# Kernel tuning notes

Measured on AMD Instinct MI355X. Metric: run time of the kernel, lower is better.

## Reference

```python
import jax, jax.numpy as jnp
import numpy as np

EPS = 1e-5
NO_ACT = 3

def _causal_conv(x, w, b, dil):
    # x: [B, Cin, T], w: [Cout, Cin, K]; left-pad by (K-1)*dil == Conv1d(pad)+Chomp1d
    pad = (w.shape[2] - 1) * dil
    y = jax.lax.conv_general_dilated(x, w, window_strides=(1,), padding=[(pad, 0)],
                                     rhs_dilation=(dil,), dimension_numbers=("NCH", "OIH", "NCH"))
    return y + b[None, :, None]

def _bn(x, g, bt, m, v):
    # eval-mode BatchNorm1d over channel dim
    return (x - m[None, :, None]) * (g / jnp.sqrt(v + EPS))[None, :, None] + bt[None, :, None]

def _block(x, w1, b1, w2, b2, g1, bt1, m1, v1, g2, bt2, m2, v2, dil, dw=None, db=None):
    out = jax.nn.relu(_bn(_causal_conv(x, w1, b1, dil), g1, bt1, m1, v1))
    out = jax.nn.relu(_bn(_causal_conv(out, w2, b2, dil), g2, bt2, m2, v2))
    res = x if dw is None else _causal_conv(x, dw, db, 1)
    return jax.nn.relu(out + res)

def _logits(x, c0w1, c0b1, c0w2, c0b2, c0g1, c0bt1, c0m1, c0v1, c0g2, c0bt2, c0m2, c0v2, c0dw, c0db,
            c1w1, c1b1, c1w2, c1b2, c1g1, c1bt1, c1m1, c1v1, c1g2, c1bt2, c1m2, c1v2, aw, ab, lw, lb):
    h = jnp.swapaxes(x, 1, 2)  # [B, Cin, T]
    h = _block(h, c0w1, c0b1, c0w2, c0b2, c0g1, c0bt1, c0m1, c0v1, c0g2, c0bt2, c0m2, c0v2, 1, c0dw, c0db)
    h = _block(h, c1w1, c1b1, c1w2, c1b2, c1g1, c1bt1, c1m1, c1v1, c1g2, c1bt2, c1m2, c1v2, 2)
    z = jnp.swapaxes(h, 1, 2)  # [B, T, C]
    attn = jax.nn.sigmoid(z @ aw + ab)  # [B, T, 1]
    return (z * attn) @ lw + lb  # [B, T, 5]

def setup_inputs():
    key = jax.random.key(0)
    ks = iter(jax.random.split(key, 64))
    B, T, CIN, C, K, NC = 32, 4096, 34, 256, 3, 5
    def conv_w(co, ci, k):
        return jax.random.normal(next(ks), (co, ci, k), jnp.float32) * np.float32(np.sqrt(2.0 / (ci * k)))
    def vec(n, kind="randn"):
        if kind == "randn":
            return jax.random.normal(next(ks), (n,), jnp.float32) * 0.1
        return jax.random.uniform(next(ks), (n,), jnp.float32, 0.5, 1.5)
    inp = {"x": jax.random.normal(next(ks), (B, T, CIN), jnp.float32)}
    for i, ci in [(0, CIN), (1, C)]:
        inp[f"c{i}w1"] = conv_w(C, ci, K); inp[f"c{i}b1"] = vec(C)
        inp[f"c{i}w2"] = conv_w(C, C, K); inp[f"c{i}b2"] = vec(C)
        for j in (1, 2):
            inp[f"c{i}g{j}"] = 1.0 + vec(C)
            inp[f"c{i}bt{j}"] = vec(C)
            inp[f"c{i}m{j}"] = vec(C)
            inp[f"c{i}v{j}"] = vec(C, "rand")
    inp["c0dw"] = conv_w(C, CIN, 1); inp["c0db"] = vec(C)
    inp["aw"] = jax.random.normal(next(ks), (C, 1), jnp.float32) * np.float32(np.sqrt(1.0 / C))
    inp["ab"] = vec(1)
    inp["lw"] = jax.random.normal(next(ks), (C, NC), jnp.float32) * np.float32(np.sqrt(1.0 / C))
    inp["lb"] = vec(NC)
    return inp

def reference(x, c0w1, c0b1, c0w2, c0b2, c0g1, c0bt1, c0m1, c0v1, c0g2, c0bt2, c0m2, c0v2, c0dw, c0db,
              c1w1, c1b1, c1w2, c1b2, c1g1, c1bt1, c1m1, c1v1, c1g2, c1bt2, c1m2, c1v2, aw, ab, lw, lb):
    logits = _logits(x, c0w1, c0b1, c0w2, c0b2, c0g1, c0bt1, c0m1, c0v1, c0g2, c0bt2, c0m2, c0v2, c0dw, c0db,
                     c1w1, c1b1, c1w2, c1b2, c1g1, c1bt1, c1m1, c1v1, c1g2, c1bt2, c1m2, c1v2, aw, ab, lw, lb)
    probs = jax.nn.softmax(logits, axis=-1)
    B, T, NC = probs.shape
    preds = jnp.argmax(probs, axis=-1).astype(jnp.int32)
    # --- conservative no-activity: clipped window (size 5) majority check ---
    non3 = (preds != NO_ACT).astype(jnp.int32)
    cs = jnp.concatenate([jnp.zeros((B, 1), jnp.int32), jnp.cumsum(non3, axis=1)], axis=1)  # [B, T+1]
    t = jnp.arange(T)
    start = jnp.maximum(0, t - 2)
    end = jnp.minimum(T, t + 3)
    wsum = cs[:, end] - cs[:, start]          # non-no-activity count in window, [B, T]
    wlen = (end - start)[None, :]
    alt = jnp.argmax(probs.at[:, :, NO_ACT].set(0.0), axis=-1).astype(jnp.int32)
    proc = jnp.where((preds == NO_ACT) & (2 * wsum > wlen), alt, preds)
    # --- transition rules: sequential state smoothing scan over time ---
    TM = jnp.ones((5, 5), jnp.float32).at[1, 2].set(0.0).at[2, 0].set(0.0)
    def step(prev, inp):
        curr, p = inp                          # curr: [B] int32, p: [B, 5]
        mask = TM[prev]                        # allowed next-states, [B, 5]
        invalid = jnp.take_along_axis(mask, curr[:, None], axis=1)[:, 0] == 0
        vp = p * mask
        cand = jnp.where(vp.sum(-1) == 0, prev, jnp.argmax(vp, axis=-1).astype(jnp.int32))
        new = jnp.where(invalid, cand, curr)
        return new, new
    init = proc[:, 0]
    _, rest = jax.lax.scan(step, init, (proc[:, 1:].T, jnp.swapaxes(probs[:, 1:], 0, 1)))
    processed = jnp.concatenate([init[:, None], rest.T], axis=1)  # [B, T]
    return logits, processed
```

## Files before the change

kernel.cpp:

```cpp
#include <hip/hip_runtime.h>
#include <hip/hip_bf16.h>


#define T_LEN 4096
#define CIN   34
#define EPSV  1e-5f
#define HALO  16
#define TT    48
#define TW    64
#define NTILE 86

__device__ __forceinline__ int hswz(int row, int col) {
    return row * TW + ((((col >> 2) ^ ((row >> 3) & 15)) << 2) | (col & 3));
}
__device__ __forceinline__ float4* lds_ptr4(float* buf, int row, int col) {
    return (float4*)&buf[row * TW + (((col >> 2) ^ ((row >> 3) & 15)) << 2)];
}
__device__ __forceinline__ float4 lds_read4(const float* buf, int row, int col) {
    return *(const float4*)&buf[row * TW + (((col >> 2) ^ ((row >> 3) & 15)) << 2)];
}

__device__ __forceinline__ void bs_load(const float* __restrict__ wraw, int ch,
                                        float4 r[3], int tid) {
    #pragma unroll
    for (int k = 0; k < 3; ++k) {
        int s = tid + k * 512;
        int co = s / 6, q = s - co * 6;
        r[k] = *(const float4*)&wraw[co * 768 + ch * 24 + q * 4];
    }
}
__device__ __forceinline__ void bs_write(float* wch, const float4 r[3], int tid) {
    #pragma unroll
    for (int k = 0; k < 3; ++k) {
        int s = tid + k * 512;
        int co = s / 6, q = s - co * 6;
        wch[(q * 4 + 0) * 256 + co] = r[k].x;
        wch[(q * 4 + 1) * 256 + co] = r[k].y;
        wch[(q * 4 + 2) * 256 + co] = r[k].z;
        wch[(q * 4 + 3) * 256 + co] = r[k].w;
    }
}

__device__ __forceinline__ void s1_load(const float* __restrict__ w1, int ch,
                                        float r[12], int tid) {
    int nrows = (ch < 4) ? 24 : 6;
    int slots = nrows * 256;
    #pragma unroll
    for (int k = 0; k < 12; ++k) {
        int s = tid + k * 512;
        if (s < slots) {
            int co = s / nrows, kr = s - co * nrows;
            r[k] = w1[co * 102 + ch * 24 + kr];
        }
    }
}
__device__ __forceinline__ void s1_write(float* wch, int ch, const float r[12], int tid) {
    int nrows = (ch < 4) ? 24 : 6;
    int slots = nrows * 256;
    #pragma unroll
    for (int k = 0; k < 12; ++k) {
        int s = tid + k * 512;
        if (s < slots) {
            int co = s / nrows, kr = s - co * nrows;
            wch[kr * 256 + co] = r[k];
        }
    }
}

__device__ __forceinline__ void ds_stage(float* wch, const float* __restrict__ dw,
                                         int ch, int tid) {
    int nci = (ch < 4) ? 8 : 2;
    int slots = nci * 256;
    #pragma unroll
    for (int k = 0; k < 4; ++k) {
        int s = tid + k * 512;
        if (s < slots) {
            int ci_l = s % nci, co = s / nci;
            wch[ci_l * 256 + co] = dw[co * CIN + ch * 8 + ci_l];
        }
    }
}

template <int DIL>
__device__ __forceinline__ void chunk_compute(const float* src, const float* wch,
                                              int rowBase, int KH, int co0, int c0,
                                              float (&acc)[8][16]) {
    const int cL = (c0 >= 4) ? c0 - 4 : 0;
    #pragma unroll
    for (int rep = 0; rep < 2; ++rep) {
        int ci_l = KH + rep * 4;
        int row = rowBase + ci_l;
        float rw[20];
        *(float4*)&rw[0]  = lds_read4(src, row, cL);
        *(float4*)&rw[4]  = lds_read4(src, row, c0);
        *(float4*)&rw[8]  = lds_read4(src, row, c0 + 4);
        *(float4*)&rw[12] = lds_read4(src, row, c0 + 8);
        *(float4*)&rw[16] = lds_read4(src, row, c0 + 12);
        #pragma unroll
        for (int kk = 0; kk < 3; ++kk) {
            float wv[8];
            *(float4*)&wv[0] = *(const float4*)&wch[(ci_l * 3 + kk) * 256 + co0];
            *(float4*)&wv[4] = *(const float4*)&wch[(ci_l * 3 + kk) * 256 + co0 + 4];
            const int off = (DIL == 2) ? 2 * kk : kk + 2;
            #pragma unroll
            for (int i = 0; i < 8; ++i)
                #pragma unroll
                for (int j = 0; j < 16; ++j)
                    acc[i][j] += wv[i] * rw[j + off];
        }
    }
}

__device__ __forceinline__ void chunk_compute_x(const float* __restrict__ x,
                                                const float* wch, int b, int t0,
                                                int ciBase, int nci, int KH,
                                                int co0, int c0, float (&acc)[8][16]) {
    #pragma unroll
    for (int rep = 0; rep < 2; ++rep) {
        int ci_l = KH + rep * 4;
        if (ci_l < nci) {
            int ci = ciBase + ci_l;
            float rw[20];
            rw[0] = 0.f; rw[1] = 0.f;
            #pragma unroll
            for (int idx = 2; idx < 20; ++idx) {
                int t = t0 - HALO + c0 + idx - 4;
                rw[idx] = (t >= 0 && t < T_LEN) ? x[(b * T_LEN + t) * CIN + ci] : 0.f;
            }
            #pragma unroll
            for (int kk = 0; kk < 3; ++kk) {
                float wv[8];
                *(float4*)&wv[0] = *(const float4*)&wch[(ci_l * 3 + kk) * 256 + co0];
                *(float4*)&wv[4] = *(const float4*)&wch[(ci_l * 3 + kk) * 256 + co0 + 4];
                #pragma unroll
                for (int i = 0; i < 8; ++i)
                    #pragma unroll
                    for (int j = 0; j < 16; ++j)
                        acc[i][j] += wv[i] * rw[j + kk + 2];
            }
        }
    }
}

__device__ __forceinline__ void chunk_compute_ds(const float* __restrict__ x,
                                                 const float* wch, int b, int t0,
                                                 int ciBase, int nci, int KH,
                                                 int co0, int c0, float (&acc)[8][16]) {
    #pragma unroll
    for (int rep = 0; rep < 2; ++rep) {
        int ci_l = KH + rep * 4;
        if (ci_l < nci) {
            int ci = ciBase + ci_l;
            float xv[16];
            #pragma unroll
            for (int j = 0; j < 16; ++j) {
                int t = t0 - HALO + c0 + j;
                xv[j] = (t >= 0 && t < T_LEN) ? x[(b * T_LEN + t) * CIN + ci] : 0.f;
            }
            float wv[8];
            *(float4*)&wv[0] = *(const float4*)&wch[ci_l * 256 + co0];
            *(float4*)&wv[4] = *(const float4*)&wch[ci_l * 256 + co0 + 4];
            #pragma unroll
            for (int i = 0; i < 8; ++i)
                #pragma unroll
                for (int j = 0; j < 16; ++j)
                    acc[i][j] += wv[i] * xv[j];
        }
    }
}

__device__ __forceinline__ void kh_store(float* tgt, float (&acc)[8][16], int co0, int c0) {
    #pragma unroll
    for (int i = 0; i < 8; ++i)
        #pragma unroll
        for (int j4 = 0; j4 < 4; ++j4)
            *lds_ptr4(tgt, co0 + i, c0 + j4 * 4) =
                make_float4(acc[i][j4*4+0], acc[i][j4*4+1], acc[i][j4*4+2], acc[i][j4*4+3]);
}
__device__ __forceinline__ void kh_add(float* tgt, float (&acc)[8][16], int co0, int c0) {
    #pragma unroll
    for (int i = 0; i < 8; ++i)
        #pragma unroll
        for (int j4 = 0; j4 < 4; ++j4) {
            float4* p = lds_ptr4(tgt, co0 + i, c0 + j4 * 4);
            float4 pv = *p;
            pv.x += acc[i][j4*4+0]; pv.y += acc[i][j4*4+1];
            pv.z += acc[i][j4*4+2]; pv.w += acc[i][j4*4+3];
            *p = pv;
        }
}
__device__ __forceinline__ void kh_final0(float* tgt, float (&acc)[8][16],
                                          const float* __restrict__ g,  const float* __restrict__ bt,
                                          const float* __restrict__ m,  const float* __restrict__ v,
                                          const float* __restrict__ bb,
                                          int co0, int c0, int t0) {
    #pragma unroll
    for (int i = 0; i < 8; ++i) {
        int co = co0 + i;
        float sc = g[co] / sqrtf(v[co] + EPSV);
        float bi = (bb[co] - m[co]) * sc + bt[co];
        #pragma unroll
        for (int j4 = 0; j4 < 4; ++j4) {
            float4* p = lds_ptr4(tgt, co, c0 + j4 * 4);
            float4 pv = *p;
            float pr[4] = {pv.x, pv.y, pv.z, pv.w};
            float o[4];
            #pragma unroll
            for (int r = 0; r < 4; ++r) {
                float s = (pr[r] + acc[i][j4*4+r]) * sc + bi;
                o[r] = fmaxf(s, 0.f);
                int t = t0 - HALO + c0 + j4 * 4 + r;
                if (t < 0) o[r] = 0.f;
            }
            *p = make_float4(o[0], o[1], o[2], o[3]);
        }
    }
}
__device__ __forceinline__ void kh_res2(float* tgt, float (&acc)[8][16],
                                        const float* __restrict__ db,
                                        int co0, int c0, int t0) {
    #pragma unroll
    for (int i = 0; i < 8; ++i) {
        float d = db[co0 + i];
        #pragma unroll
        for (int j4 = 0; j4 < 4; ++j4) {
            float4* p = lds_ptr4(tgt, co0 + i, c0 + j4 * 4);
            float4 pv = *p;
            float pr[4] = {pv.x, pv.y, pv.z, pv.w};
            float o[4];
            #pragma unroll
            for (int r = 0; r < 4; ++r) {
                float s = pr[r] + acc[i][j4*4+r] + d;
                o[r] = fmaxf(s, 0.f);
                int t = t0 - HALO + c0 + j4 * 4 + r;
                if (t < 0) o[r] = 0.f;
            }
            *p = make_float4(o[0], o[1], o[2], o[3]);
        }
    }
}

#define ZERO_ACC() { _Pragma("unroll") for (int i = 0; i < 8; ++i) \
                     _Pragma("unroll") for (int j = 0; j < 16; ++j) acc[i][j] = 0.f; }

#define REDUCE0(TGT, G, BT, M, V, BB) {                         \
    __syncthreads();                                            \
    if (KH == 3) kh_store(TGT, acc, co0, c0);                   \
    __syncthreads();                                            \
    if (KH == 2) kh_add(TGT, acc, co0, c0);                     \
    __syncthreads();                                            \
    if (KH == 1) kh_add(TGT, acc, co0, c0);                     \
    __syncthreads();                                            \
    if (KH == 0) kh_final0(TGT, acc, G, BT, M, V, BB, co0, c0, t0); \
    __syncthreads(); }

#define REDUCE_RES(TGT, DB) {                                   \
    __syncthreads();                                            \
    if (KH == 3) kh_add(TGT, acc, co0, c0);                     \
    __syncthreads();                                            \
    if (KH == 2) kh_add(TGT, acc, co0, c0);                     \
    __syncthreads();                                            \
    if (KH == 1) kh_add(TGT, acc, co0, c0);                     \
    __syncthreads();                                            \
    if (KH == 0) kh_res2(TGT, acc, DB, co0, c0, t0);            \
    __syncthreads(); }

__global__ __launch_bounds__(512, 2) void tcn_fused(
    const float* __restrict__ x,
    const float* __restrict__ c0w1, const float* __restrict__ c0b1,
    const float* __restrict__ c0w2, const float* __restrict__ c0b2,
    const float* __restrict__ c0g1, const float* __restrict__ c0bt1,
    const float* __restrict__ c0m1, const float* __restrict__ c0v1,
    const float* __restrict__ c0g2, const float* __restrict__ c0bt2,
    const float* __restrict__ c0m2, const float* __restrict__ c0v2,
    const float* __restrict__ c1w1, const float* __restrict__ c1b1,
    const float* __restrict__ c1w2, const float* __restrict__ c1b2,
    const float* __restrict__ c1g1, const float* __restrict__ c1bt1,
    const float* __restrict__ c1m1, const float* __restrict__ c1v1,
    const float* __restrict__ c1g2, const float* __restrict__ c1bt2,
    const float* __restrict__ c1m2, const float* __restrict__ c1v2,
    const float* __restrict__ c0dw, const float* __restrict__ c0db,
    const float* __restrict__ aw,   const float* __restrict__ ab,
    const float* __restrict__ lw,   const float* __restrict__ lb,
    float* __restrict__ out)
{
    __shared__ float bufA[256 * TW];
    __shared__ float bufB[256 * TW];
    __shared__ float wch[24 * 256];

    const int b   = blockIdx.y;
    const int t0  = blockIdx.x * TT;
    const int tid = threadIdx.x;
    const int CG  = tid & 31, sg = tid >> 5;
    const int TG  = sg & 3,  KH = sg >> 2;
    const int co0 = CG * 8,  c0 = TG * 16;

    float acc[8][16];

    ZERO_ACC();
    {
        float r[12];
        s1_load(c0w1, 0, r, tid);
        for (int ch = 0; ch < 5; ++ch) {
            __syncthreads();
            s1_write(wch, ch, r, tid);
            __syncthreads();
            if (ch + 1 < 5) s1_load(c0w1, ch + 1, r, tid);
            chunk_compute_x(x, wch, b, t0, ch * 8, (ch < 4) ? 8 : 2, KH, co0, c0, acc);
        }
    }
    REDUCE0(bufA, c0g1, c0bt1, c0m1, c0v1, c0b1);

    ZERO_ACC();
    {
        float4 r4[3];
        bs_load(c0w2, 0, r4, tid);
        for (int ch = 0; ch < 32; ++ch) {
            __syncthreads();
            bs_write(wch, r4, tid);
            __syncthreads();
            if (ch + 1 < 32) bs_load(c0w2, ch + 1, r4, tid);
            chunk_compute<1>(bufA, wch, ch * 8, KH, co0, c0, acc);
        }
    }
    REDUCE0(bufB, c0g2, c0bt2, c0m2, c0v2, c0b2);

    ZERO_ACC();
    for (int ch = 0; ch < 5; ++ch) {
        __syncthreads();
        ds_stage(wch, c0dw, ch, tid);
        __syncthreads();
        chunk_compute_ds(x, wch, b, t0, ch * 8, (ch < 4) ? 8 : 2, KH, co0, c0, acc);
    }
    REDUCE_RES(bufB, c0db);

    ZERO_ACC();
    {
        float4 r4[3];
        bs_load(c1w1, 0, r4, tid);
        for (int ch = 0; ch < 32; ++ch) {
            __syncthreads();
            bs_write(wch, r4, tid);
            __syncthreads();
            if (ch + 1 < 32) bs_load(c1w1, ch + 1, r4, tid);
            chunk_compute<2>(bufB, wch, ch * 8, KH, co0, c0, acc);
        }
    }
    REDUCE0(bufA, c1g1, c1bt1, c1m1, c1v1, c1b1);

    ZERO_ACC();
    {
        float4 r4[3];
        bs_load(c1w2, 0, r4, tid);
        for (int ch = 0; ch < 32; ++ch) {
            __syncthreads();
            bs_write(wch, r4, tid);
            __syncthreads();
            if (ch + 1 < 32) bs_load(c1w2, ch + 1, r4, tid);
            chunk_compute<2>(bufA, wch, ch * 8, KH, co0, c0, acc);
        }
    }
    REDUCE0(bufA, c1g2, c1bt2, c1m2, c1v2, c1b2);

    {
        #pragma unroll
        for (int ii = 0; ii < 2; ++ii) {
            int co = co0 + KH * 2 + ii;
            #pragma unroll
            for (int j4 = 0; j4 < 4; ++j4) {
                float4* p = lds_ptr4(bufA, co, c0 + j4 * 4);
                float4 a = *p;
                float4 rr = lds_read4(bufB, co, c0 + j4 * 4);
                a.x = fmaxf(a.x + rr.x, 0.f);
                a.y = fmaxf(a.y + rr.y, 0.f);
                a.z = fmaxf(a.z + rr.z, 0.f);
                a.w = fmaxf(a.w + rr.w, 0.f);
                *p = a;
            }
        }
    }
    __syncthreads();

    for (int s = tid; s < 1542; s += 512) {
        float vput;
        if (s < 256)       vput = aw[s];
        else if (s < 1536) vput = lw[s - 256];
        else if (s == 1536) vput = ab[0];
        else               vput = lb[s - 1537];
        wch[s] = vput;
    }
    __syncthreads();
    {
        int col = tid >> 3, oct = tid & 7;
        if (col >= HALO) {
            int t = t0 - HALO + col;
            float s1 = 0.f, s5[5] = {0.f, 0.f, 0.f, 0.f, 0.f};
            for (int q = 0; q < 32; ++q) {
                int co = oct * 32 + q;
                float z = bufA[hswz(co, col)];
                s1 += z * wch[co];
                #pragma unroll
                for (int nc = 0; nc < 5; ++nc) s5[nc] += z * wch[256 + co * 5 + nc];
            }
            #pragma unroll
            for (int mm = 1; mm <= 4; mm <<= 1) {
                s1 += __shfl_xor(s1, mm, 64);
                #pragma unroll
                for (int nc = 0; nc < 5; ++nc) s5[nc] += __shfl_xor(s5[nc], mm, 64);
            }
            if (oct == 0 && t < T_LEN) {
                float at = 1.f / (1.f + expf(-(s1 + wch[1536])));
                float* dst = &out[(b * T_LEN + t) * 5];
                #pragma unroll
                for (int nc = 0; nc < 5; ++nc) dst[nc] = at * s5[nc] + wch[1537 + nc];
            }
        }
    }
}

__global__ __launch_bounds__(256) void postproc(
    const float* __restrict__ logits, float* __restrict__ outp)
{
    const int b = blockIdx.x;
    const int tid = threadIdx.x;
    __shared__ signed char preds[4096], alt3[4096], ax2[4096], ax0[4096],
                           proc[4096], resa[4096];

    for (int t = tid; t < T_LEN; t += 256) {
        const float* p = &logits[(b * T_LEN + t) * 5];
        float l0 = p[0], l1 = p[1], l2 = p[2], l3 = p[3], l4 = p[4];
        int am = 0; float mv = l0;
        if (l1 > mv) { am = 1; mv = l1; }
        if (l2 > mv) { am = 2; mv = l2; }
        if (l3 > mv) { am = 3; mv = l3; }
        if (l4 > mv) { am = 4; mv = l4; }
        int a3 = 0; float m3 = l0;
        if (l1 > m3) { a3 = 1; m3 = l1; }
        if (l2 > m3) { a3 = 2; m3 = l2; }
        if (l4 > m3) { a3 = 4; }
        int a2 = 0; float m2 = l0;
        if (l1 > m2) { a2 = 1; m2 = l1; }
        if (l3 > m2) { a2 = 3; m2 = l3; }
        if (l4 > m2) { a2 = 4; }
        int a0 = 1; float m0 = l1;
        if (l2 > m0) { a0 = 2; m0 = l2; }
        if (l3 > m0) { a0 = 3; m0 = l3; }
        if (l4 > m0) { a0 = 4; }
        preds[t] = (signed char)am;
        alt3[t]  = (signed char)a3;
        ax2[t]   = (signed char)a2;
        ax0[t]   = (signed char)a0;
    }
    __syncthreads();
    for (int t = tid; t < T_LEN; t += 256) {
        int s0 = t - 2 > 0 ? t - 2 : 0;
        int e0 = t + 3 < T_LEN ? t + 3 : T_LEN;
        int wsum = 0;
        for (int s = s0; s < e0; ++s) wsum += (preds[s] != 3);
        int wl = e0 - s0;
        int pd = preds[t];
        proc[t] = (pd == 3 && 2 * wsum > wl) ? alt3[t] : (signed char)pd;
    }
    __syncthreads();
    if (tid == 0) {
        int p = proc[0];
        resa[0] = (signed char)p;
        for (int t = 1; t < T_LEN; ++t) {
            int c = proc[t];
            int n = c;
            if (p == 1 && c == 2) n = ax2[t];
            else if (p == 2 && c == 0) n = ax0[t];
            resa[t] = (signed char)n;
            p = n;
        }
    }
    __syncthreads();
    for (int t = tid; t < T_LEN; t += 256) outp[b * T_LEN + t] = (float)resa[t];
}

extern "C" void kernel_launch(void* const* d_in, const int* in_sizes, int n_in,
                              void* d_out, int out_size, void* d_ws, size_t ws_size,
                              hipStream_t stream)
{
    const float* x     = (const float*)d_in[0];
    const float* c0w1  = (const float*)d_in[1];
    const float* c0b1  = (const float*)d_in[2];
    const float* c0w2  = (const float*)d_in[3];
    const float* c0b2  = (const float*)d_in[4];
    const float* c0g1  = (const float*)d_in[5];
    const float* c0bt1 = (const float*)d_in[6];
    const float* c0m1  = (const float*)d_in[7];
    const float* c0v1  = (const float*)d_in[8];
    const float* c0g2  = (const float*)d_in[9];
    const float* c0bt2 = (const float*)d_in[10];
    const float* c0m2  = (const float*)d_in[11];
    const float* c0v2  = (const float*)d_in[12];
    const float* c1w1  = (const float*)d_in[13];
    const float* c1b1  = (const float*)d_in[14];
    const float* c1w2  = (const float*)d_in[15];
    const float* c1b2  = (const float*)d_in[16];
    const float* c1g1  = (const float*)d_in[17];
    const float* c1bt1 = (const float*)d_in[18];
    const float* c1m1  = (const float*)d_in[19];
    const float* c1v1  = (const float*)d_in[20];
    const float* c1g2  = (const float*)d_in[21];
    const float* c1bt2 = (const float*)d_in[22];
    const float* c1m2  = (const float*)d_in[23];
    const float* c1v2  = (const float*)d_in[24];
    const float* c0dw  = (const float*)d_in[25];
    const float* c0db  = (const float*)d_in[26];
    const float* aw    = (const float*)d_in[27];
    const float* ab    = (const float*)d_in[28];
    const float* lw    = (const float*)d_in[29];
    const float* lb    = (const float*)d_in[30];

    float* logits = (float*)d_out;

    tcn_fused<<<dim3(NTILE, 32), 512, 0, stream>>>(
        x,
        c0w1, c0b1, c0w2, c0b2,
        c0g1, c0bt1, c0m1, c0v1,
        c0g2, c0bt2, c0m2, c0v2,
        c1w1, c1b1, c1w2, c1b2,
        c1g1, c1bt1, c1m1, c1v1,
        c1g2, c1bt2, c1m2, c1v2,
        c0dw, c0db, aw, ab, lw, lb,
        logits);

    postproc<<<32, 256, 0, stream>>>(logits, ((float*)d_out) + 32 * 4096 * 5);
}
```

Measured before the change: 5.066 ms.

## Pre-transpose weights to workspace and read them from global instead of LDS staging

A prep kernel transposes all conv weights into a co-contiguous layout in workspace, so the fused TCN kernel reads weights straight from global/L2 rather than staging chunks through LDS with many barriers. Each thread now owns an 8x4 output tile and loops over input channels split four ways within its own registers, which removes the LDS cross-group reduction. LDS drops to one activation buffer plus an input tile, allowing four blocks per CU. The trade-off is more global weight traffic per FMA (8 weights per 32 FMAs) and an extra launch.

```diff
diff --git a/kernel.cpp b/kernel.cpp
--- a/kernel.cpp
+++ b/kernel.cpp
@@ -10,6 +10,13 @@
 #define TW    64
 #define NTILE 86
 
+#define WOFF_WT1 0
+#define WOFF_WT2 26112
+#define WOFF_WT3 222720
+#define WOFF_WT4 419328
+#define WOFF_WTD 615936
+#define WS_FLOATS 624640
+
 __device__ __forceinline__ int hswz(int row, int col) {
     return row * TW + ((((col >> 2) ^ ((row >> 3) & 15)) << 2) | (col & 3));
 }
@@ -20,374 +27,275 @@
     return *(const float4*)&buf[row * TW + (((col >> 2) ^ ((row >> 3) & 15)) << 2)];
 }
 
-__device__ __forceinline__ void bs_load(const float* __restrict__ wraw, int ch,
-                                        float4 r[3], int tid) {
-    #pragma unroll
-    for (int k = 0; k < 3; ++k) {
-        int s = tid + k * 512;
-        int co = s / 6, q = s - co * 6;
-        r[k] = *(const float4*)&wraw[co * 768 + ch * 24 + q * 4];
-    }
-}
-__device__ __forceinline__ void bs_write(float* wch, const float4 r[3], int tid) {
-    #pragma unroll
-    for (int k = 0; k < 3; ++k) {
-        int s = tid + k * 512;
-        int co = s / 6, q = s - co * 6;
-        wch[(q * 4 + 0) * 256 + co] = r[k].x;
-        wch[(q * 4 + 1) * 256 + co] = r[k].y;
-        wch[(q * 4 + 2) * 256 + co] = r[k].z;
-        wch[(q * 4 + 3) * 256 + co] = r[k].w;
-    }
-}
-
-__device__ __forceinline__ void s1_load(const float* __restrict__ w1, int ch,
-                                        float r[12], int tid) {
-    int nrows = (ch < 4) ? 24 : 6;
-    int slots = nrows * 256;
-    #pragma unroll
-    for (int k = 0; k < 12; ++k) {
-        int s = tid + k * 512;
-        if (s < slots) {
-            int co = s / nrows, kr = s - co * nrows;
-            r[k] = w1[co * 102 + ch * 24 + kr];
-        }
-    }
-}
-__device__ __forceinline__ void s1_write(float* wch, int ch, const float r[12], int tid) {
-    int nrows = (ch < 4) ? 24 : 6;
-    int slots = nrows * 256;
-    #pragma unroll
-    for (int k = 0; k < 12; ++k) {
-        int s = tid + k * 512;
-        if (s < slots) {
-            int co = s / nrows, kr = s - co * nrows;
-            wch[kr * 256 + co] = r[k];
-        }
-    }
-}
-
-__device__ __forceinline__ void ds_stage(float* wch, const float* __restrict__ dw,
-                                         int ch, int tid) {
-    int nci = (ch < 4) ? 8 : 2;
-    int slots = nci * 256;
-    #pragma unroll
-    for (int k = 0; k < 4; ++k) {
-        int s = tid + k * 512;
-        if (s < slots) {
-            int ci_l = s % nci, co = s / nci;
-            wch[ci_l * 256 + co] = dw[co * CIN + ch * 8 + ci_l];
-        }
-    }
-}
-
-template <int DIL>
-__device__ __forceinline__ void chunk_compute(const float* src, const float* wch,
-                                              int rowBase, int KH, int co0, int c0,
-                                              float (&acc)[8][16]) {
-    const int cL = (c0 >= 4) ? c0 - 4 : 0;
-    #pragma unroll
-    for (int rep = 0; rep < 2; ++rep) {
-        int ci_l = KH + rep * 4;
-        int row = rowBase + ci_l;
-        float rw[20];
-        *(float4*)&rw[0]  = lds_read4(src, row, cL);
-        *(float4*)&rw[4]  = lds_read4(src, row, c0);
-        *(float4*)&rw[8]  = lds_read4(src, row, c0 + 4);
-        *(float4*)&rw[12] = lds_read4(src, row, c0 + 8);
-        *(float4*)&rw[16] = lds_read4(src, row, c0 + 12);
+__global__ __launch_bounds__(256) void prep_v3(
+    const float* __restrict__ c0w1, const float* __restrict__ c0w2,
+    const float* __restrict__ c1w1, const float* __restrict__ c1w2,
+    const float* __restrict__ c0dw, float* __restrict__ ws)
+{
+    int idx = blockIdx.x * 256 + threadIdx.x;
+    if (idx < 26112) {
+        int co = idx & 255, r = idx >> 8, ci = r / 3, kk = r % 3;
+        ws[WOFF_WT1 + idx] = c0w1[(co * CIN + ci) * 3 + kk];
+        return;
+    }
+    idx -= 26112;
+    if (idx < 196608) {
+        int co = idx & 255, r = idx >> 8, ci = r / 3, kk = r % 3;
+        ws[WOFF_WT2 + idx] = c0w2[(co * 256 + ci) * 3 + kk];
+        return;
+    }
+    idx -= 196608;
+    if (idx < 196608) {
+        int co = idx & 255, r = idx >> 8, ci = r / 3, kk = r % 3;
+        ws[WOFF_WT3 + idx] = c1w1[(co * 256 + ci) * 3 + kk];
+        return;
+    }
+    idx -= 196608;
+    if (idx < 196608) {
+        int co = idx & 255, r = idx >> 8, ci = r / 3, kk = r % 3;
+        ws[WOFF_WT4 + idx] = c1w2[(co * 256 + ci) * 3 + kk];
+        return;
+    }
+    idx -= 196608;
+    if (idx < 8704) {
+        int co = idx & 255, ci = idx >> 8;
+        ws[WOFF_WTD + idx] = c0dw[co * CIN + ci];
+    }
+}
+
+__device__ __forceinline__ void bzero8(float (&bk)[8][4]) {
+    #pragma unroll
+    for (int i = 0; i < 8; ++i)
+        #pragma unroll
+        for (int j = 0; j < 4; ++j) bk[i][j] = 0.f;
+}
+__device__ __forceinline__ void badd8(float (&A)[8][4], const float (&B)[8][4]) {
+    #pragma unroll
+    for (int i = 0; i < 8; ++i)
+        #pragma unroll
+        for (int j = 0; j < 4; ++j) A[i][j] = A[i][j] + B[i][j];
+}
+
+__device__ __forceinline__ void sweep_s1(const float* xs, const float* __restrict__ WT,
+                                         int r, int c0, int co0, float (&bk)[8][4]) {
+    bzero8(bk);
+    for (int ci = r; ci < CIN; ci += 4) {
+        float rw[6];
+        #pragma unroll
+        for (int q = 0; q < 6; ++q) rw[q] = xs[ci * 69 + c0 + 2 + q];
         #pragma unroll
         for (int kk = 0; kk < 3; ++kk) {
             float wv[8];
-            *(float4*)&wv[0] = *(const float4*)&wch[(ci_l * 3 + kk) * 256 + co0];
-            *(float4*)&wv[4] = *(const float4*)&wch[(ci_l * 3 + kk) * 256 + co0 + 4];
+            *(float4*)&wv[0] = *(const float4*)&WT[(ci * 3 + kk) * 256 + co0];
+            *(float4*)&wv[4] = *(const float4*)&WT[(ci * 3 + kk) * 256 + co0 + 4];
+            #pragma unroll
+            for (int i = 0; i < 8; ++i)
+                #pragma unroll
+                for (int j = 0; j < 4; ++j)
+                    bk[i][j] += wv[i] * rw[j + kk];
+        }
+    }
+}
+
+template <int DIL>
+__device__ __forceinline__ void sweep_cv(const float* bufH, const float* __restrict__ WT,
+                                         int r, int c0, int cL, int co0, float (&bk)[8][4]) {
+    bzero8(bk);
+    for (int ci = r; ci < 256; ci += 4) {
+        float rw[8];
+        *(float4*)&rw[0] = lds_read4(bufH, ci, cL);
+        *(float4*)&rw[4] = lds_read4(bufH, ci, c0);
+        #pragma unroll
+        for (int kk = 0; kk < 3; ++kk) {
+            float wv[8];
+            *(float4*)&wv[0] = *(const float4*)&WT[(ci * 3 + kk) * 256 + co0];
+            *(float4*)&wv[4] = *(const float4*)&WT[(ci * 3 + kk) * 256 + co0 + 4];
             const int off = (DIL == 2) ? 2 * kk : kk + 2;
             #pragma unroll
             for (int i = 0; i < 8; ++i)
                 #pragma unroll
-                for (int j = 0; j < 16; ++j)
-                    acc[i][j] += wv[i] * rw[j + off];
-        }
-    }
-}
-
-__device__ __forceinline__ void chunk_compute_x(const float* __restrict__ x,
-                                                const float* wch, int b, int t0,
-                                                int ciBase, int nci, int KH,
-                                                int co0, int c0, float (&acc)[8][16]) {
-    #pragma unroll
-    for (int rep = 0; rep < 2; ++rep) {
-        int ci_l = KH + rep * 4;
-        if (ci_l < nci) {
-            int ci = ciBase + ci_l;
-            float rw[20];
-            rw[0] = 0.f; rw[1] = 0.f;
+                for (int j = 0; j < 4; ++j)
+                    bk[i][j] += wv[i] * rw[j + off];
+        }
+    }
+}
+
+__device__ __forceinline__ void sweep_ds(const float* xs, const float* __restrict__ WTD,
+                                         int r, int c0, int co0, float (&bk)[8][4]) {
+    bzero8(bk);
+    for (int ci = r; ci < CIN; ci += 4) {
+        float xv[4];
+        #pragma unroll
+        for (int q = 0; q < 4; ++q) xv[q] = xs[ci * 69 + c0 + 4 + q];
+        float wv[8];
+        *(float4*)&wv[0] = *(const float4*)&WTD[ci * 256 + co0];
+        *(float4*)&wv[4] = *(const float4*)&WTD[ci * 256 + co0 + 4];
+        #pragma unroll
+        for (int i = 0; i < 8; ++i)
             #pragma unroll
-            for (int idx = 2; idx < 20; ++idx) {
-                int t = t0 - HALO + c0 + idx - 4;
-                rw[idx] = (t >= 0 && t < T_LEN) ? x[(b * T_LEN + t) * CIN + ci] : 0.f;
-            }
-            #pragma unroll
-            for (int kk = 0; kk < 3; ++kk) {
-                float wv[8];
-                *(float4*)&wv[0] = *(const float4*)&wch[(ci_l * 3 + kk) * 256 + co0];
-                *(float4*)&wv[4] = *(const float4*)&wch[(ci_l * 3 + kk) * 256 + co0 + 4];
-                #pragma unroll
-                for (int i = 0; i < 8; ++i)
-                    #pragma unroll
-                    for (int j = 0; j < 16; ++j)
-                        acc[i][j] += wv[i] * rw[j + kk + 2];
-            }
-        }
-    }
-}
-
-__device__ __forceinline__ void chunk_compute_ds(const float* __restrict__ x,
-                                                 const float* wch, int b, int t0,
-                                                 int ciBase, int nci, int KH,
-                                                 int co0, int c0, float (&acc)[8][16]) {
-    #pragma unroll
-    for (int rep = 0; rep < 2; ++rep) {
-        int ci_l = KH + rep * 4;
-        if (ci_l < nci) {
-            int ci = ciBase + ci_l;
-            float xv[16];
-            #pragma unroll
-            for (int j = 0; j < 16; ++j) {
-                int t = t0 - HALO + c0 + j;
-                xv[j] = (t >= 0 && t < T_LEN) ? x[(b * T_LEN + t) * CIN + ci] : 0.f;
-            }
-            float wv[8];
-            *(float4*)&wv[0] = *(const float4*)&wch[ci_l * 256 + co0];
-            *(float4*)&wv[4] = *(const float4*)&wch[ci_l * 256 + co0 + 4];
-            #pragma unroll
-            for (int i = 0; i < 8; ++i)
-                #pragma unroll
-                for (int j = 0; j < 16; ++j)
-                    acc[i][j] += wv[i] * xv[j];
-        }
-    }
-}
-
-__device__ __forceinline__ void kh_store(float* tgt, float (&acc)[8][16], int co0, int c0) {
-    #pragma unroll
-    for (int i = 0; i < 8; ++i)
-        #pragma unroll
-        for (int j4 = 0; j4 < 4; ++j4)
-            *lds_ptr4(tgt, co0 + i, c0 + j4 * 4) =
-                make_float4(acc[i][j4*4+0], acc[i][j4*4+1], acc[i][j4*4+2], acc[i][j4*4+3]);
-}
-__device__ __forceinline__ void kh_add(float* tgt, float (&acc)[8][16], int co0, int c0) {
-    #pragma unroll
-    for (int i = 0; i < 8; ++i)
-        #pragma unroll
-        for (int j4 = 0; j4 < 4; ++j4) {
-            float4* p = lds_ptr4(tgt, co0 + i, c0 + j4 * 4);
-            float4 pv = *p;
-            pv.x += acc[i][j4*4+0]; pv.y += acc[i][j4*4+1];
-            pv.z += acc[i][j4*4+2]; pv.w += acc[i][j4*4+3];
-            *p = pv;
-        }
-}
-__device__ __forceinline__ void kh_final0(float* tgt, float (&acc)[8][16],
-                                          const float* __restrict__ g,  const float* __restrict__ bt,
-                                          const float* __restrict__ m,  const float* __restrict__ v,
-                                          const float* __restrict__ bb,
-                                          int co0, int c0, int t0) {
-    #pragma unroll
-    for (int i = 0; i < 8; ++i) {
-        int co = co0 + i;
-        float sc = g[co] / sqrtf(v[co] + EPSV);
-        float bi = (bb[co] - m[co]) * sc + bt[co];
-        #pragma unroll
-        for (int j4 = 0; j4 < 4; ++j4) {
-            float4* p = lds_ptr4(tgt, co, c0 + j4 * 4);
-            float4 pv = *p;
-            float pr[4] = {pv.x, pv.y, pv.z, pv.w};
-            float o[4];
-            #pragma unroll
-            for (int r = 0; r < 4; ++r) {
-                float s = (pr[r] + acc[i][j4*4+r]) * sc + bi;
-                o[r] = fmaxf(s, 0.f);
-                int t = t0 - HALO + c0 + j4 * 4 + r;
-                if (t < 0) o[r] = 0.f;
-            }
-            *p = make_float4(o[0], o[1], o[2], o[3]);
-        }
-    }
-}
-__device__ __forceinline__ void kh_res2(float* tgt, float (&acc)[8][16],
-                                        const float* __restrict__ db,
-                                        int co0, int c0, int t0) {
-    #pragma unroll
-    for (int i = 0; i < 8; ++i) {
-        float d = db[co0 + i];
-        #pragma unroll
-        for (int j4 = 0; j4 < 4; ++j4) {
-            float4* p = lds_ptr4(tgt, co0 + i, c0 + j4 * 4);
-            float4 pv = *p;
-            float pr[4] = {pv.x, pv.y, pv.z, pv.w};
-            float o[4];
-            #pragma unroll
-            for (int r = 0; r < 4; ++r) {
-                float s = pr[r] + acc[i][j4*4+r] + d;
-                o[r] = fmaxf(s, 0.f);
-                int t = t0 - HALO + c0 + j4 * 4 + r;
-                if (t < 0) o[r] = 0.f;
-            }
-            *p = make_float4(o[0], o[1], o[2], o[3]);
-        }
-    }
-}
-
-#define ZERO_ACC() { _Pragma("unroll") for (int i = 0; i < 8; ++i) \
-                     _Pragma("unroll") for (int j = 0; j < 16; ++j) acc[i][j] = 0.f; }
-
-#define REDUCE0(TGT, G, BT, M, V, BB) {                         \
-    __syncthreads();                                            \
-    if (KH == 3) kh_store(TGT, acc, co0, c0);                   \
-    __syncthreads();                                            \
-    if (KH == 2) kh_add(TGT, acc, co0, c0);                     \
-    __syncthreads();                                            \
-    if (KH == 1) kh_add(TGT, acc, co0, c0);                     \
-    __syncthreads();                                            \
-    if (KH == 0) kh_final0(TGT, acc, G, BT, M, V, BB, co0, c0, t0); \
-    __syncthreads(); }
-
-#define REDUCE_RES(TGT, DB) {                                   \
-    __syncthreads();                                            \
-    if (KH == 3) kh_add(TGT, acc, co0, c0);                     \
-    __syncthreads();                                            \
-    if (KH == 2) kh_add(TGT, acc, co0, c0);                     \
-    __syncthreads();                                            \
-    if (KH == 1) kh_add(TGT, acc, co0, c0);                     \
-    __syncthreads();                                            \
-    if (KH == 0) kh_res2(TGT, acc, DB, co0, c0, t0);            \
-    __syncthreads(); }
-
-__global__ __launch_bounds__(512, 2) void tcn_fused(
-    const float* __restrict__ x,
-    const float* __restrict__ c0w1, const float* __restrict__ c0b1,
-    const float* __restrict__ c0w2, const float* __restrict__ c0b2,
-    const float* __restrict__ c0g1, const float* __restrict__ c0bt1,
-    const float* __restrict__ c0m1, const float* __restrict__ c0v1,
-    const float* __restrict__ c0g2, const float* __restrict__ c0bt2,
-    const float* __restrict__ c0m2, const float* __restrict__ c0v2,
-    const float* __restrict__ c1w1, const float* __restrict__ c1b1,
-    const float* __restrict__ c1w2, const float* __restrict__ c1b2,
-    const float* __restrict__ c1g1, const float* __restrict__ c1bt1,
-    const float* __restrict__ c1m1, const float* __restrict__ c1v1,
-    const float* __restrict__ c1g2, const float* __restrict__ c1bt2,
-    const float* __restrict__ c1m2, const float* __restrict__ c1v2,
-    const float* __restrict__ c0dw, const float* __restrict__ c0db,
-    const float* __restrict__ aw,   const float* __restrict__ ab,
-    const float* __restrict__ lw,   const float* __restrict__ lb,
+            for (int j = 0; j < 4; ++j)
+                bk[i][j] += wv[i] * xv[j];
+    }
+}
+
+__global__ __launch_bounds__(512, 4) void tcn_v5(
+    const float* __restrict__ x,  const float* __restrict__ ws,
+    const float* __restrict__ c0b1, const float* __restrict__ c0g1,
+    const float* __restrict__ c0bt1, const float* __restrict__ c0m1, const float* __restrict__ c0v1,
+    const float* __restrict__ c0b2, const float* __restrict__ c0g2,
+    const float* __restrict__ c0bt2, const float* __restrict__ c0m2, const float* __restrict__ c0v2,
+    const float* __restrict__ c1b1, const float* __restrict__ c1g1,
+    const float* __restrict__ c1bt1, const float* __restrict__ c1m1, const float* __restrict__ c1v1,
+    const float* __restrict__ c1b2, const float* __restrict__ c1g2,
+    const float* __restrict__ c1bt2, const float* __restrict__ c1m2, const float* __restrict__ c1v2,
+    const float* __restrict__ c0db,
+    const float* __restrict__ aw, const float* __restrict__ ab,
+    const float* __restrict__ lw, const float* __restrict__ lb,
     float* __restrict__ out)
 {
-    __shared__ float bufA[256 * TW];
-    __shared__ float bufB[256 * TW];
-    __shared__ float wch[24 * 256];
+    __shared__ float bufH[256 * TW];
+    __shared__ float xs[34 * 69];
 
     const int b   = blockIdx.y;
     const int t0  = blockIdx.x * TT;
     const int tid = threadIdx.x;
-    const int CG  = tid & 31, sg = tid >> 5;
-    const int TG  = sg & 3,  KH = sg >> 2;
-    const int co0 = CG * 8,  c0 = TG * 16;
-
-    float acc[8][16];
-
-    ZERO_ACC();
-    {
-        float r[12];
-        s1_load(c0w1, 0, r, tid);
-        for (int ch = 0; ch < 5; ++ch) {
-            __syncthreads();
-            s1_write(wch, ch, r, tid);
-            __syncthreads();
-            if (ch + 1 < 5) s1_load(c0w1, ch + 1, r, tid);
-            chunk_compute_x(x, wch, b, t0, ch * 8, (ch < 4) ? 8 : 2, KH, co0, c0, acc);
-        }
-    }
-    REDUCE0(bufA, c0g1, c0bt1, c0m1, c0v1, c0b1);
-
-    ZERO_ACC();
-    {
-        float4 r4[3];
-        bs_load(c0w2, 0, r4, tid);
-        for (int ch = 0; ch < 32; ++ch) {
-            __syncthreads();
-            bs_write(wch, r4, tid);
-            __syncthreads();
-            if (ch + 1 < 32) bs_load(c0w2, ch + 1, r4, tid);
-            chunk_compute<1>(bufA, wch, ch * 8, KH, co0, c0, acc);
-        }
-    }
-    REDUCE0(bufB, c0g2, c0bt2, c0m2, c0v2, c0b2);
-
-    ZERO_ACC();
-    for (int ch = 0; ch < 5; ++ch) {
-        __syncthreads();
-        ds_stage(wch, c0dw, ch, tid);
-        __syncthreads();
-        chunk_compute_ds(x, wch, b, t0, ch * 8, (ch < 4) ? 8 : 2, KH, co0, c0, acc);
-    }
-    REDUCE_RES(bufB, c0db);
-
-    ZERO_ACC();
-    {
-        float4 r4[3];
-        bs_load(c1w1, 0, r4, tid);
-        for (int ch = 0; ch < 32; ++ch) {
-            __syncthreads();
-            bs_write(wch, r4, tid);
-            __syncthreads();
-            if (ch + 1 < 32) bs_load(c1w1, ch + 1, r4, tid);
-            chunk_compute<2>(bufB, wch, ch * 8, KH, co0, c0, acc);
-        }
-    }
-    REDUCE0(bufA, c1g1, c1bt1, c1m1, c1v1, c1b1);
-
-    ZERO_ACC();
-    {
-        float4 r4[3];
-        bs_load(c1w2, 0, r4, tid);
-        for (int ch = 0; ch < 32; ++ch) {
-            __syncthreads();
-            bs_write(wch, r4, tid);
-            __syncthreads();
-            if (ch + 1 < 32) bs_load(c1w2, ch + 1, r4, tid);
-            chunk_compute<2>(bufA, wch, ch * 8, KH, co0, c0, acc);
-        }
-    }
-    REDUCE0(bufA, c1g2, c1bt2, c1m2, c1v2, c1b2);
-
-    {
-        #pragma unroll
-        for (int ii = 0; ii < 2; ++ii) {
-            int co = co0 + KH * 2 + ii;
-            #pragma unroll
-            for (int j4 = 0; j4 < 4; ++j4) {
-                float4* p = lds_ptr4(bufA, co, c0 + j4 * 4);
-                float4 a = *p;
-                float4 rr = lds_read4(bufB, co, c0 + j4 * 4);
-                a.x = fmaxf(a.x + rr.x, 0.f);
-                a.y = fmaxf(a.y + rr.y, 0.f);
-                a.z = fmaxf(a.z + rr.z, 0.f);
-                a.w = fmaxf(a.w + rr.w, 0.f);
-                *p = a;
-            }
-        }
-    }
+    const int CG  = tid >> 4, TG = tid & 15;
+    const int co0 = CG * 8,  c0 = TG * 4;
+    const int cL  = (c0 >= 4) ? c0 - 4 : 0;
+
+    const float* WT1 = ws + WOFF_WT1;
+    const float* WT2 = ws + WOFF_WT2;
+    const float* WT3 = ws + WOFF_WT3;
+    const float* WT4 = ws + WOFF_WT4;
+    const float* WTD = ws + WOFF_WTD;
+
+    for (int s = tid; s < 34 * 68; s += 512) {
+        int ci = s % 34, col = s / 34;
+        int t = t0 - 20 + col;
+        xs[ci * 69 + col] = (t >= 0 && t < T_LEN) ? x[(b * T_LEN + t) * CIN + ci] : 0.f;
+    }
+    __syncthreads();
+
+    float B1[8][4], B2[8][4], hr[8][4];
+
+    sweep_s1(xs, WT1, 3, c0, co0, B1);
+    sweep_s1(xs, WT1, 2, c0, co0, B2); badd8(B1, B2);
+    sweep_s1(xs, WT1, 1, c0, co0, B2); badd8(B1, B2);
+    sweep_s1(xs, WT1, 0, c0, co0, B2);
+    #pragma unroll
+    for (int i = 0; i < 8; ++i) {
+        int co = co0 + i;
+        float sc = c0g1[co] / sqrtf(c0v1[co] + EPSV);
+        float bi = (c0b1[co] - c0m1[co]) * sc + c0bt1[co];
+        #pragma unroll
+        for (int j = 0; j < 4; ++j) {
+            float s = (B1[i][j] + B2[i][j]) * sc + bi;
+            float ov = fmaxf(s, 0.f);
+            int t = t0 - HALO + c0 + j;
+            if (t < 0) ov = 0.f;
+            B1[i][j] = ov;
+        }
+    }
+    #pragma unroll
+    for (int i = 0; i < 8; ++i)
+        *lds_ptr4(bufH, co0 + i, c0) = make_float4(B1[i][0], B1[i][1], B1[i][2], B1[i][3]);
+    __syncthreads();
+
+    sweep_cv<1>(bufH, WT2, 3, c0, cL, co0, B1);
+    sweep_cv<1>(bufH, WT2, 2, c0, cL, co0, B2); badd8(B1, B2);
+    sweep_cv<1>(bufH, WT2, 1, c0, cL, co0, B2); badd8(B1, B2);
+    sweep_cv<1>(bufH, WT2, 0, c0, cL, co0, B2);
+    #pragma unroll
+    for (int i = 0; i < 8; ++i) {
+        int co = co0 + i;
+        float sc = c0g2[co] / sqrtf(c0v2[co] + EPSV);
+        float bi = (c0b2[co] - c0m2[co]) * sc + c0bt2[co];
+        #pragma unroll
+        for (int j = 0; j < 4; ++j) {
+            float s = (B1[i][j] + B2[i][j]) * sc + bi;
+            float ov = fmaxf(s, 0.f);
+            int t = t0 - HALO + c0 + j;
+            if (t < 0) ov = 0.f;
+            hr[i][j] = ov;
+        }
+    }
+    sweep_ds(xs, WTD, 3, c0, co0, B1); badd8(hr, B1);
+    sweep_ds(xs, WTD, 2, c0, co0, B1); badd8(hr, B1);
+    sweep_ds(xs, WTD, 1, c0, co0, B1); badd8(hr, B1);
+    sweep_ds(xs, WTD, 0, c0, co0, B1);
+    #pragma unroll
+    for (int i = 0; i < 8; ++i) {
+        float d = c0db[co0 + i];
+        #pragma unroll
+        for (int j = 0; j < 4; ++j) {
+            float s = hr[i][j] + B1[i][j] + d;
+            float ov = fmaxf(s, 0.f);
+            int t = t0 - HALO + c0 + j;
+            if (t < 0) ov = 0.f;
+            hr[i][j] = ov;
+        }
+    }
+    __syncthreads();
+    #pragma unroll
+    for (int i = 0; i < 8; ++i)
+        *lds_ptr4(bufH, co0 + i, c0) = make_float4(hr[i][0], hr[i][1], hr[i][2], hr[i][3]);
+    __syncthreads();
+
+    sweep_cv<2>(bufH, WT3, 3, c0, cL, co0, B1);
+    sweep_cv<2>(bufH, WT3, 2, c0, cL, co0, B2); badd8(B1, B2);
+    sweep_cv<2>(bufH, WT3, 1, c0, cL, co0, B2); badd8(B1, B2);
+    sweep_cv<2>(bufH, WT3, 0, c0, cL, co0, B2);
+    #pragma unroll
+    for (int i = 0; i < 8; ++i) {
+        int co = co0 + i;
+        float sc = c1g1[co] / sqrtf(c1v1[co] + EPSV);
+        float bi = (c1b1[co] - c1m1[co]) * sc + c1bt1[co];
+        #pragma unroll
+        for (int j = 0; j < 4; ++j) {
+            float s = (B1[i][j] + B2[i][j]) * sc + bi;
+            float ov = fmaxf(s, 0.f);
+            int t = t0 - HALO + c0 + j;
+            if (t < 0) ov = 0.f;
+            B1[i][j] = ov;
+        }
+    }
+    __syncthreads();
+    #pragma unroll
+    for (int i = 0; i < 8; ++i)
+        *lds_ptr4(bufH, co0 + i, c0) = make_float4(B1[i][0], B1[i][1], B1[i][2], B1[i][3]);
+    __syncthreads();
+
+    sweep_cv<2>(bufH, WT4, 3, c0, cL, co0, B1);
+    sweep_cv<2>(bufH, WT4, 2, c0, cL, co0, B2); badd8(B1, B2);
+    sweep_cv<2>(bufH, WT4, 1, c0, cL, co0, B2); badd8(B1, B2);
+    sweep_cv<2>(bufH, WT4, 0, c0, cL, co0, B2);
+    #pragma unroll
+    for (int i = 0; i < 8; ++i) {
+        int co = co0 + i;
+        float sc = c1g2[co] / sqrtf(c1v2[co] + EPSV);
+        float bi = (c1b2[co] - c1m2[co]) * sc + c1bt2[co];
+        #pragma unroll
+        for (int j = 0; j < 4; ++j) {
+            float s = (B1[i][j] + B2[i][j]) * sc + bi;
+            float a = fmaxf(s, 0.f);
+            int t = t0 - HALO + c0 + j;
+            if (t < 0) a = 0.f;
+            B1[i][j] = fmaxf(a + hr[i][j], 0.f);
+        }
+    }
+    __syncthreads();
+    #pragma unroll
+    for (int i = 0; i < 8; ++i)
+        *lds_ptr4(bufH, co0 + i, c0) = make_float4(B1[i][0], B1[i][1], B1[i][2], B1[i][3]);
     __syncthreads();
 
     for (int s = tid; s < 1542; s += 512) {
         float vput;
-        if (s < 256)       vput = aw[s];
-        else if (s < 1536) vput = lw[s - 256];
+        if (s < 256)        vput = aw[s];
+        else if (s < 1536)  vput = lw[s - 256];
         else if (s == 1536) vput = ab[0];
-        else               vput = lb[s - 1537];
-        wch[s] = vput;
+        else                vput = lb[s - 1537];
+        xs[s] = vput;
     }
     __syncthreads();
     {
@@ -397,10 +305,10 @@
             float s1 = 0.f, s5[5] = {0.f, 0.f, 0.f, 0.f, 0.f};
             for (int q = 0; q < 32; ++q) {
                 int co = oct * 32 + q;
-                float z = bufA[hswz(co, col)];
-                s1 += z * wch[co];
+                float z = bufH[hswz(co, col)];
+                s1 += z * xs[co];
                 #pragma unroll
-                for (int nc = 0; nc < 5; ++nc) s5[nc] += z * wch[256 + co * 5 + nc];
+                for (int nc = 0; nc < 5; ++nc) s5[nc] += z * xs[256 + co * 5 + nc];
             }
             #pragma unroll
             for (int mm = 1; mm <= 4; mm <<= 1) {
@@ -409,10 +317,10 @@
                 for (int nc = 0; nc < 5; ++nc) s5[nc] += __shfl_xor(s5[nc], mm, 64);
             }
             if (oct == 0 && t < T_LEN) {
-                float at = 1.f / (1.f + expf(-(s1 + wch[1536])));
+                float at = 1.f / (1.f + expf(-(s1 + xs[1536])));
                 float* dst = &out[(b * T_LEN + t) * 5];
                 #pragma unroll
-                for (int nc = 0; nc < 5; ++nc) dst[nc] = at * s5[nc] + wch[1537 + nc];
+                for (int nc = 0; nc < 5; ++nc) dst[nc] = at * s5[nc] + xs[1537 + nc];
             }
         }
     }
@@ -515,17 +423,15 @@
     const float* lb    = (const float*)d_in[30];
 
     float* logits = (float*)d_out;
-
-    tcn_fused<<<dim3(NTILE, 32), 512, 0, stream>>>(
-        x,
-        c0w1, c0b1, c0w2, c0b2,
-        c0g1, c0bt1, c0m1, c0v1,
-        c0g2, c0bt2, c0m2, c0v2,
-        c1w1, c1b1, c1w2, c1b2,
-        c1g1, c1bt1, c1m1, c1v1,
-        c1g2, c1bt2, c1m2, c1v2,
-        c0dw, c0db, aw, ab, lw, lb,
-        logits);
-
+    float* ws = (float*)d_ws;
+
+    prep_v3<<<2440, 256, 0, stream>>>(c0w1, c0w2, c1w1, c1w2, c0dw, ws);
+    tcn_v5<<<dim3(NTILE, 32), 512, 0, stream>>>(
+        x, ws,
+        c0b1, c0g1, c0bt1, c0m1, c0v1,
+        c0b2, c0g2, c0bt2, c0m2, c0v2,
+        c1b1, c1g1, c1bt1, c1m1, c1v1,
+        c1b2, c1g2, c1bt2, c1m2, c1v2,
+        c0db, aw, ab, lw, lb, logits);
     postproc<<<32, 256, 0, stream>>>(logits, ((float*)d_out) + 32 * 4096 * 5);
 }
```

After: 4.484 ms. 11.5% less time.
